# Kernel tuning notes

Measured on AMD Instinct MI355X. Metric: run time of the kernel, lower is better.

Reference implementation:

```python
import jax, jax.numpy as jnp
import numpy as np

EPS = 1e-6
SCALE_END = 1.0


def _rms_norm(x, w):
    # x: [B, L, H, D], w: [D]
    var = jnp.mean(jnp.square(x), axis=-1, keepdims=True)
    return x * jax.lax.rsqrt(var + EPS) * w


def _apply_rope(x, freqs):
    # x: [B, L, H, D]; freqs: [L, D//2] rotation angles.
    # Interleaved pair rotation: (x0, x1) -> (x0*cos - x1*sin, x0*sin + x1*cos)
    B, L, H, D = x.shape
    xr = x.reshape(B, L, H, D // 2, 2)
    x0, x1 = xr[..., 0], xr[..., 1]
    cos = jnp.cos(freqs)[None, :, None, :]  # [1, L, 1, D//2]
    sin = jnp.sin(freqs)[None, :, None, :]
    o0 = x0 * cos - x1 * sin
    o1 = x0 * sin + x1 * cos
    return jnp.stack([o0, o1], axis=-1).reshape(B, L, H, D)


def setup_inputs() -> dict:
    key = jax.random.key(0)
    ks = jax.random.split(key, 6)
    B, Lq, Lk, H, D = 1, 4096, 1024, 24, 128
    hidden = H * D
    query = jax.random.normal(ks[0], (B, Lq, H, D), dtype=jnp.float32)
    ref_latent = jax.random.normal(ks[1], (B, Lk, hidden), dtype=jnp.float32)
    ref_freqs = jax.random.uniform(ks[2], (Lk, D // 2), dtype=jnp.float32)
    Wk = jax.random.normal(ks[3], (hidden, hidden), dtype=jnp.float32) * (hidden ** -0.5)
    Wv = jax.random.normal(ks[4], (hidden, hidden), dtype=jnp.float32) * (hidden ** -0.5)
    rms_w = jnp.ones((D,), dtype=jnp.float32)
    return {"query": query, "ref_latent": ref_latent, "ref_freqs": ref_freqs,
            "Wk": Wk, "Wv": Wv, "rms_w": rms_w}


def reference(query, ref_latent, ref_freqs, Wk, Wv, rms_w):
    B, Lq, H, D = query.shape
    # K/V projections (nn.Linear: y = x @ W.T)
    ref_k = jnp.einsum('ble,he->blh', ref_latent, Wk).reshape(B, -1, H, D)
    ref_v = jnp.einsum('ble,he->blh', ref_latent, Wv).reshape(B, -1, H, D)
    # RMSNorm on K heads, then rotary embedding on K
    ref_k = _rms_norm(ref_k, rms_w)
    ref_k = _apply_rope(ref_k, ref_freqs)
    # Non-causal attention, softmax_scale = head_dim ** -0.5 (flash_attn layout B L H D)
    scale = D ** -0.5
    scores = jnp.einsum('bqhd,bkhd->bhqk', query, ref_k) * scale
    probs = jax.nn.softmax(scores, axis=-1)
    attn = jnp.einsum('bhqk,bkhd->bqhd', probs, ref_v)
    attn = attn.reshape(B, Lq, H * D)
    return SCALE_END * attn
```

## Files before the change

### kernel.cpp

```cpp
#include <hip/hip_runtime.h>
#include <hip/hip_bf16.h>

typedef __attribute__((ext_vector_type(8))) short short8;
typedef float floatx4 __attribute__((ext_vector_type(4)));
typedef float floatx16 __attribute__((ext_vector_type(16)));

#define LQ 4096
#define LK 1024
#define NH 24
#define HD 128
#define HID 3072

__device__ __forceinline__ unsigned short f2bf(float f) {
    __hip_bfloat16 h = __float2bfloat16(f);
    union { __hip_bfloat16 b; unsigned short u; } c; c.b = h;
    return c.u;
}

__device__ __forceinline__ unsigned cvtpk(float a, float b) {
    unsigned r;
    asm("v_cvt_pk_bf16_f32 %0, %1, %2" : "=v"(r) : "v"(a), "v"(b));
    return r;
}

__device__ __forceinline__ float fexp2(float x) {
    float r;
    asm("v_exp_f32 %0, %1" : "=v"(r) : "v"(x));
    return r;
}

__device__ __forceinline__ void gload16(const void* g, void* l) {
    __builtin_amdgcn_global_load_lds(
        (const __attribute__((address_space(1))) void*)g,
        (__attribute__((address_space(3))) void*)l,
        16, 0, 0);
}

__global__ void cvt_all(const float* __restrict__ latent, const float* __restrict__ Wk,
                        const float* __restrict__ Wv, unsigned short* __restrict__ lbf,
                        unsigned short* __restrict__ wkbf, unsigned short* __restrict__ wvbf) {
    const int n1 = (LK * HID) / 4;
    const int n2 = (HID * HID) / 4;
    const int total = n1 + 2 * n2;
    int i = blockIdx.x * blockDim.x + threadIdx.x;
    int stride = gridDim.x * blockDim.x;
    for (; i < total; i += stride) {
        const float4* src; ushort4* dst; int j;
        if (i < n1)            { src = (const float4*)latent; dst = (ushort4*)lbf;  j = i; }
        else if (i < n1 + n2)  { src = (const float4*)Wk;     dst = (ushort4*)wkbf; j = i - n1; }
        else                   { src = (const float4*)Wv;     dst = (ushort4*)wvbf; j = i - n1 - n2; }
        float4 v = src[j];
        ushort4 o;
        o.x = f2bf(v.x); o.y = f2bf(v.y); o.z = f2bf(v.z); o.w = f2bf(v.w);
        dst[j] = o;
    }
}

__global__ __launch_bounds__(256) void gemm_fused(const unsigned short* __restrict__ A,
                                                  const unsigned short* __restrict__ Bw,
                                                  const float* __restrict__ freqs,
                                                  const float* __restrict__ rmsw,
                                                  unsigned short* __restrict__ Out,
                                                  int mode) {
    __shared__ __align__(16) unsigned short As[2][32 * 64];
    __shared__ __align__(16) unsigned short Bs[2][128 * 64];
    __shared__ float redK[32][4];
    const int tid = threadIdx.x;
    const int lane = tid & 63;
    const int wave = tid >> 6;
    const int flat = blockIdx.x;
    const int wid = (flat & 7) * 96 + (flat >> 3);
    const int lt = wid & 31;
    const int h  = wid >> 5;
    const int bm0 = lt * 32;
    const int bn0 = h * 128;
    const int lr = lane & 15;
    const int lg = lane >> 4;

    floatx4 acc[2][2];
    for (int i = 0; i < 2; ++i)
        for (int j = 0; j < 2; ++j)
            acc[i][j] = (floatx4){0.f, 0.f, 0.f, 0.f};

    auto stage = [&](int b, int k0) {
        {
            int r = tid >> 3, cb = tid & 7;
            int g = cb ^ (r & 7);
            gload16(&A[(bm0 + r) * HID + k0 + g * 8], &As[b][(wave * 64) * 8]);
        }
        for (int p = 0; p < 4; ++p) {
            int slot = p * 256 + tid;
            int r = slot >> 3, cb = slot & 7;
            int g = cb ^ (r & 7);
            gload16(&Bw[(bn0 + r) * HID + k0 + g * 8], &Bs[b][(p * 256 + wave * 64) * 8]);
        }
    };

    auto compute = [&](int b) {
        for (int ks = 0; ks < 2; ++ks) {
            short8 af[2], bfr[2];
            for (int mt = 0; mt < 2; ++mt) {
                int m = mt * 16 + lr;
                int sc = (ks * 4 + lg) ^ (m & 7);
                af[mt] = *(const short8*)(&As[b][m * 64 + sc * 8]);
            }
            for (int nt = 0; nt < 2; ++nt) {
                int n = wave * 32 + nt * 16 + lr;
                int sc = (ks * 4 + lg) ^ (n & 7);
                bfr[nt] = *(const short8*)(&Bs[b][n * 64 + sc * 8]);
            }
            __builtin_amdgcn_s_setprio(1);
            for (int mt = 0; mt < 2; ++mt)
                for (int nt = 0; nt < 2; ++nt)
                    acc[mt][nt] = __builtin_amdgcn_mfma_f32_16x16x32_bf16(af[mt], bfr[nt], acc[mt][nt], 0, 0, 0);
            __builtin_amdgcn_s_setprio(0);
        }
    };

    stage(0, 0);
    __syncthreads();
    int buf = 0;
    for (int k0 = 0; k0 < HID - 64; k0 += 64) {
        stage(buf ^ 1, k0 + 64);
        compute(buf);
        __syncthreads();
        buf ^= 1;
    }
    compute(buf);

    if (mode == 0) {
        float part[2][4];
        for (int mt = 0; mt < 2; ++mt)
            for (int rg = 0; rg < 4; ++rg) {
                float v0 = acc[mt][0][rg], v1 = acc[mt][1][rg];
                float s = v0 * v0 + v1 * v1;
                s += __shfl_xor(s, 1);
                s += __shfl_xor(s, 2);
                s += __shfl_xor(s, 4);
                s += __shfl_xor(s, 8);
                part[mt][rg] = s;
            }
        if (lr == 0)
            for (int mt = 0; mt < 2; ++mt)
                for (int rg = 0; rg < 4; ++rg)
                    redK[mt * 16 + lg * 4 + rg][wave] = part[mt][rg];
        __syncthreads();
        for (int mt = 0; mt < 2; ++mt)
            for (int rg = 0; rg < 4; ++rg) {
                int row = mt * 16 + lg * 4 + rg;
                float tot = (redK[row][0] + redK[row][1]) + (redK[row][2] + redK[row][3]);
                float rsn = rsqrtf(tot * (1.0f / 128.0f) + 1e-6f);
                int l = bm0 + row;
                for (int nt = 0; nt < 2; ++nt) {
                    int d = wave * 32 + nt * 16 + lr;
                    float xn = acc[mt][nt][rg] * rsn * rmsw[d];
                    float f = freqs[l * (HD / 2) + (d >> 1)];
                    float sn = __sinf(f), cs = __cosf(f);
                    float partner = __shfl_xor(xn, 1);
                    float o = (d & 1) ? (partner * sn + xn * cs) : (xn * cs - partner * sn);
                    Out[l * HID + bn0 + d] = f2bf(o);
                }
            }
    } else {
        __syncthreads();
        float* Ct = (float*)&Bs[0][0];
        for (int mt = 0; mt < 2; ++mt)
            for (int nt = 0; nt < 2; ++nt)
                for (int rg = 0; rg < 4; ++rg)
                    Ct[(mt * 16 + lg * 4 + rg) * 132 + wave * 32 + nt * 16 + lr] = acc[mt][nt][rg];
        __syncthreads();
        unsigned short* dst = Out + (((size_t)(h * 32 + lt)) << 12);
        for (int p = 0; p < 2; ++p) {
            int slot = p * 256 + tid;
            int l31v = slot & 31;
            int hi2 = (slot >> 5) & 1;
            int c2 = (slot >> 6) & 1;
            int ntd = slot >> 7;
            int col = ntd * 32 + l31v;
            int r0 = c2 * 16 + hi2 * 8;
            short8 v;
            for (int j = 0; j < 8; ++j)
                v[j] = (short)f2bf(Ct[(r0 + j) * 132 + col]);
            *(short8*)(&dst[slot * 8]) = v;
        }
    }
}

__global__ __launch_bounds__(256, 3) void attn(const float* __restrict__ Q,
                                               const unsigned short* __restrict__ Kbf,
                                               const unsigned short* __restrict__ Vfrag,
                                               float* __restrict__ O) {
    __shared__ __align__(16) unsigned short KA[2][32 * 128];
    __shared__ __align__(16) unsigned short KB[2][32 * 128];
    __shared__ __align__(16) unsigned short VA[32 * 128];
    __shared__ __align__(16) unsigned short VB[32 * 128];
    const int tid = threadIdx.x;
    const int lane = tid & 63;
    const int wave = tid >> 6;
    const int l31 = lane & 31;
    const int hi = lane >> 5;
    const int flat = blockIdx.x + gridDim.x * blockIdx.y;
    const int wid = (flat & 7) * 96 + (flat >> 3);
    const int h = wid >> 5;
    const int q0 = (wid & 31) * 128 + wave * 32;
    const float qscale = 0.08838834764831843f * 1.44269504088896340736f;
    const float SHIFT = 32.0f;

    short8 qf[8];
#pragma unroll
    for (int m = 0; m < 8; ++m) {
        const float* qp = &Q[(q0 + l31) * HID + h * HD + m * 16 + hi * 8];
        float4 lo = *(const float4*)(qp);
        float4 hif = *(const float4*)(qp + 4);
        short8 v;
        v[0] = (short)f2bf(lo.x * qscale);
        v[1] = (short)f2bf(lo.y * qscale);
        v[2] = (short)f2bf(lo.z * qscale);
        v[3] = (short)f2bf(lo.w * qscale);
        v[4] = (short)f2bf(hif.x * qscale);
        v[5] = (short)f2bf(hif.y * qscale);
        v[6] = (short)f2bf(hif.z * qscale);
        v[7] = (short)f2bf(hif.w * qscale);
        qf[m] = v;
    }

    floatx16 accO[4];
#pragma unroll
    for (int i = 0; i < 4; ++i)
#pragma unroll
        for (int r = 0; r < 16; ++r) accO[i][r] = 0.f;
    float psum = 0.f;

    auto stageK = [&](unsigned short* dst, int kt) {
        for (int i = 0; i < 2; ++i) {
            int slot = i * 256 + tid;
            int r = slot >> 4, bb = slot & 15;
            int g = bb ^ (r & 15);
            gload16(&Kbf[(kt * 32 + r) * HID + h * HD + g * 8],
                    &dst[(i * 256 + wave * 64) * 8]);
        }
    };
    auto stageV = [&](unsigned short* dst, int kt) {
        const unsigned short* src = Vfrag + ((size_t)(h * 32 + kt) << 12);
        for (int i = 0; i < 2; ++i) {
            int slot = i * 256 + tid;
            gload16(&src[slot * 8], &dst[(i * 256 + wave * 64) * 8]);
        }
    };

    auto softmax32 = [&](floatx16 s, short8& pa, short8& pb) {
        float e[16];
#pragma unroll
        for (int r = 0; r < 16; ++r) e[r] = fexp2(s[r]);
        {
            float s01 = e[0] + e[1],   s23 = e[2] + e[3];
            float s45 = e[4] + e[5],   s67 = e[6] + e[7];
            float s89 = e[8] + e[9],   sab = e[10] + e[11];
            float scd = e[12] + e[13], sef = e[14] + e[15];
            float t0 = s01 + s23, t1 = s45 + s67, t2 = s89 + sab, t3 = scd + sef;
            psum += (t0 + t1) + (t2 + t3);
        }
        unsigned d0 = cvtpk(e[0], e[1]),   d1 = cvtpk(e[2], e[3]);
        unsigned d2 = cvtpk(e[4], e[5]),   d3 = cvtpk(e[6], e[7]);
        unsigned d4 = cvtpk(e[8], e[9]),   d5 = cvtpk(e[10], e[11]);
        unsigned d6 = cvtpk(e[12], e[13]), d7 = cvtpk(e[14], e[15]);
        asm volatile("v_permlane32_swap_b32 %0, %1" : "+v"(d0), "+v"(d2));
        asm volatile("v_permlane32_swap_b32 %0, %1" : "+v"(d1), "+v"(d3));
        asm volatile("v_permlane32_swap_b32 %0, %1" : "+v"(d4), "+v"(d6));
        asm volatile("v_permlane32_swap_b32 %0, %1" : "+v"(d5), "+v"(d7));
        union { unsigned u[4]; short8 s; } p0, p1;
        p0.u[0] = d0; p0.u[1] = d1; p0.u[2] = d2; p0.u[3] = d3;
        p1.u[0] = d4; p1.u[1] = d5; p1.u[2] = d6; p1.u[3] = d7;
        pa = p0.s; pb = p1.s;
    };

    stageK(KA[0], 0);
    stageK(KB[0], 16);
    asm volatile("s_waitcnt vmcnt(0)" ::: "memory");
    __builtin_amdgcn_s_barrier();

    for (int t = 0; t < 16; ++t) {
        stageV(VA, t);
        stageV(VB, t + 16);
        if (t < 15) {
            stageK(KA[(t + 1) & 1], t + 1);
            stageK(KB[(t + 1) & 1], t + 17);
        }
        floatx16 sA, sB;
#pragma unroll
        for (int r = 0; r < 16; ++r) { sA[r] = -SHIFT; sB[r] = -SHIFT; }
        __builtin_amdgcn_s_setprio(1);
#pragma unroll
        for (int m = 0; m < 8; ++m) {
            int slot = l31 * 16 + ((m * 2 + hi) ^ (l31 & 15));
            short8 kfa = *(const short8*)(&KA[t & 1][slot * 8]);
            short8 kfb = *(const short8*)(&KB[t & 1][slot * 8]);
            sA = __builtin_amdgcn_mfma_f32_32x32x16_bf16(kfa, qf[m], sA, 0, 0, 0);
            sB = __builtin_amdgcn_mfma_f32_32x32x16_bf16(kfb, qf[m], sB, 0, 0, 0);
        }
        __builtin_amdgcn_s_setprio(0);
        short8 pA0, pA1, pB0, pB1;
        softmax32(sA, pA0, pA1);
        softmax32(sB, pB0, pB1);
        __syncthreads();
        __builtin_amdgcn_s_setprio(1);
#pragma unroll
        for (int ntd = 0; ntd < 4; ++ntd) {
            int s0 = ((ntd * 2 + 0) * 2 + hi) * 32 + l31;
            int s1 = ((ntd * 2 + 1) * 2 + hi) * 32 + l31;
            short8 vA0 = *(const short8*)(&VA[s0 * 8]);
            short8 vA1 = *(const short8*)(&VA[s1 * 8]);
            short8 vB0 = *(const short8*)(&VB[s0 * 8]);
            short8 vB1 = *(const short8*)(&VB[s1 * 8]);
            accO[ntd] = __builtin_amdgcn_mfma_f32_32x32x16_bf16(pA0, vA0, accO[ntd], 0, 0, 0);
            accO[ntd] = __builtin_amdgcn_mfma_f32_32x32x16_bf16(pA1, vA1, accO[ntd], 0, 0, 0);
            accO[ntd] = __builtin_amdgcn_mfma_f32_32x32x16_bf16(pB0, vB0, accO[ntd], 0, 0, 0);
            accO[ntd] = __builtin_amdgcn_mfma_f32_32x32x16_bf16(pB1, vB1, accO[ntd], 0, 0, 0);
        }
        __builtin_amdgcn_s_setprio(0);
        __syncthreads();
    }

    float s = psum + __shfl_xor(psum, 32);
    float rinv = 1.0f / s;
    float ri[16];
#pragma unroll
    for (int r = 0; r < 16; ++r) {
        int row = (r & 3) + 8 * (r >> 2) + 4 * hi;
        ri[r] = __shfl(rinv, row);
    }
#pragma unroll
    for (int ntd = 0; ntd < 4; ++ntd)
#pragma unroll
        for (int r = 0; r < 16; ++r) {
            int row = (r & 3) + 8 * (r >> 2) + 4 * hi;
            O[(q0 + row) * HID + h * HD + ntd * 32 + l31] = accO[ntd][r] * ri[r];
        }
}

extern "C" void kernel_launch(void* const* d_in, const int* in_sizes, int n_in,
                              void* d_out, int out_size, void* d_ws, size_t ws_size,
                              hipStream_t stream) {
    const float* Q      = (const float*)d_in[0];
    const float* latent = (const float*)d_in[1];
    const float* freqs  = (const float*)d_in[2];
    const float* Wk     = (const float*)d_in[3];
    const float* Wv     = (const float*)d_in[4];
    const float* rmsw   = (const float*)d_in[5];
    float* out = (float*)d_out;
    char* ws = (char*)d_ws;

    unsigned short* latent_bf = (unsigned short*)(ws);
    unsigned short* Wk_bf     = (unsigned short*)(ws + 6291456);
    unsigned short* Wv_bf     = (unsigned short*)(ws + 25165824);
    unsigned short* Kbf       = (unsigned short*)(ws + 44040192);
    unsigned short* Vfrag     = (unsigned short*)(ws + 50331648);

    cvt_all<<<2048, 256, 0, stream>>>(latent, Wk, Wv, latent_bf, Wk_bf, Wv_bf);
    gemm_fused<<<768, 256, 0, stream>>>(latent_bf, Wk_bf, freqs, rmsw, Kbf, 0);
    gemm_fused<<<768, 256, 0, stream>>>(latent_bf, Wv_bf, freqs, rmsw, Vfrag, 1);
    attn<<<dim3(LQ / 128, NH), 256, 0, stream>>>(Q, Kbf, Vfrag, out);
}
```

Before: 163.8 us.

## Merge K and V projection GEMMs into one launch with 64x128 tiles

Replaces the two separate projection GEMM launches with a single kernel whose blockIdx.y selects the K or V weight. The block tile grows from 32x128 to 64x128, with a 2x2 wave layout where each wave computes 32x64, which raises arithmetic intensity per LDS load. The epilogues are adapted to the larger tile, and the V fragment store now writes two 32-row tiles. This cuts one launch and improves data reuse, at the cost of more LDS and registers per block and half as many blocks per projection.

Measured after the change: 134.6 us (median of 3 runs). 1.22x faster.

```diff
diff --git a/kernel.cpp b/kernel.cpp
--- a/kernel.cpp
+++ b/kernel.cpp
@@ -56,62 +56,69 @@
     }
 }
 
-__global__ __launch_bounds__(256) void gemm_fused(const unsigned short* __restrict__ A,
-                                                  const unsigned short* __restrict__ Bw,
+__global__ __launch_bounds__(256) void proj_fused(const unsigned short* __restrict__ A,
+                                                  const unsigned short* __restrict__ WkB,
+                                                  const unsigned short* __restrict__ WvB,
                                                   const float* __restrict__ freqs,
                                                   const float* __restrict__ rmsw,
-                                                  unsigned short* __restrict__ Out,
-                                                  int mode) {
-    __shared__ __align__(16) unsigned short As[2][32 * 64];
-    __shared__ __align__(16) unsigned short Bs[2][128 * 64];
-    __shared__ float redK[32][4];
+                                                  unsigned short* __restrict__ Kbf,
+                                                  unsigned short* __restrict__ Vfrag) {
+    __shared__ __align__(16) unsigned short sh[24576];
     const int tid = threadIdx.x;
     const int lane = tid & 63;
     const int wave = tid >> 6;
+    const int wm = wave >> 1, wn = wave & 1;
+    const int mode = blockIdx.y;
     const int flat = blockIdx.x;
-    const int wid = (flat & 7) * 96 + (flat >> 3);
-    const int lt = wid & 31;
-    const int h  = wid >> 5;
-    const int bm0 = lt * 32;
+    const int wid = (flat & 7) * 48 + (flat >> 3);
+    const int lt = wid & 15;
+    const int h  = wid >> 4;
+    const int bm0 = lt * 64;
     const int bn0 = h * 128;
     const int lr = lane & 15;
     const int lg = lane >> 4;
-
-    floatx4 acc[2][2];
+    const unsigned short* Bw = mode ? WvB : WkB;
+
+    floatx4 acc[2][4];
     for (int i = 0; i < 2; ++i)
-        for (int j = 0; j < 2; ++j)
+        for (int j = 0; j < 4; ++j)
             acc[i][j] = (floatx4){0.f, 0.f, 0.f, 0.f};
 
     auto stage = [&](int b, int k0) {
-        {
-            int r = tid >> 3, cb = tid & 7;
+        unsigned short* Asb = sh + b * 4096;
+        unsigned short* Bsb = sh + 8192 + b * 8192;
+        for (int p = 0; p < 2; ++p) {
+            int slot = p * 256 + tid;
+            int r = slot >> 3, cb = slot & 7;
             int g = cb ^ (r & 7);
-            gload16(&A[(bm0 + r) * HID + k0 + g * 8], &As[b][(wave * 64) * 8]);
+            gload16(&A[(bm0 + r) * HID + k0 + g * 8], &Asb[(p * 256 + wave * 64) * 8]);
         }
         for (int p = 0; p < 4; ++p) {
             int slot = p * 256 + tid;
             int r = slot >> 3, cb = slot & 7;
             int g = cb ^ (r & 7);
-            gload16(&Bw[(bn0 + r) * HID + k0 + g * 8], &Bs[b][(p * 256 + wave * 64) * 8]);
+            gload16(&Bw[(bn0 + r) * HID + k0 + g * 8], &Bsb[(p * 256 + wave * 64) * 8]);
         }
     };
 
     auto compute = [&](int b) {
+        const unsigned short* Asb = sh + b * 4096;
+        const unsigned short* Bsb = sh + 8192 + b * 8192;
         for (int ks = 0; ks < 2; ++ks) {
-            short8 af[2], bfr[2];
+            short8 af[2], bfr[4];
             for (int mt = 0; mt < 2; ++mt) {
-                int m = mt * 16 + lr;
+                int m = wm * 32 + mt * 16 + lr;
                 int sc = (ks * 4 + lg) ^ (m & 7);
-                af[mt] = *(const short8*)(&As[b][m * 64 + sc * 8]);
+                af[mt] = *(const short8*)(&Asb[m * 64 + sc * 8]);
             }
-            for (int nt = 0; nt < 2; ++nt) {
-                int n = wave * 32 + nt * 16 + lr;
+            for (int nt = 0; nt < 4; ++nt) {
+                int n = wn * 64 + nt * 16 + lr;
                 int sc = (ks * 4 + lg) ^ (n & 7);
-                bfr[nt] = *(const short8*)(&Bs[b][n * 64 + sc * 8]);
+                bfr[nt] = *(const short8*)(&Bsb[n * 64 + sc * 8]);
             }
             __builtin_amdgcn_s_setprio(1);
             for (int mt = 0; mt < 2; ++mt)
-                for (int nt = 0; nt < 2; ++nt)
+                for (int nt = 0; nt < 4; ++nt)
                     acc[mt][nt] = __builtin_amdgcn_mfma_f32_16x16x32_bf16(af[mt], bfr[nt], acc[mt][nt], 0, 0, 0);
             __builtin_amdgcn_s_setprio(0);
         }
@@ -127,61 +134,62 @@
         buf ^= 1;
     }
     compute(buf);
+    __syncthreads();
 
     if (mode == 0) {
-        float part[2][4];
+        float* red = (float*)sh;
         for (int mt = 0; mt < 2; ++mt)
             for (int rg = 0; rg < 4; ++rg) {
-                float v0 = acc[mt][0][rg], v1 = acc[mt][1][rg];
-                float s = v0 * v0 + v1 * v1;
+                float s = 0.f;
+                for (int nt = 0; nt < 4; ++nt) {
+                    float v = acc[mt][nt][rg];
+                    s += v * v;
+                }
                 s += __shfl_xor(s, 1);
                 s += __shfl_xor(s, 2);
                 s += __shfl_xor(s, 4);
                 s += __shfl_xor(s, 8);
-                part[mt][rg] = s;
+                if (lr == 0) red[(wm * 32 + mt * 16 + lg * 4 + rg) * 2 + wn] = s;
             }
-        if (lr == 0)
-            for (int mt = 0; mt < 2; ++mt)
-                for (int rg = 0; rg < 4; ++rg)
-                    redK[mt * 16 + lg * 4 + rg][wave] = part[mt][rg];
         __syncthreads();
         for (int mt = 0; mt < 2; ++mt)
             for (int rg = 0; rg < 4; ++rg) {
-                int row = mt * 16 + lg * 4 + rg;
-                float tot = (redK[row][0] + redK[row][1]) + (redK[row][2] + redK[row][3]);
+                int row = wm * 32 + mt * 16 + lg * 4 + rg;
+                float tot = red[row * 2] + red[row * 2 + 1];
                 float rsn = rsqrtf(tot * (1.0f / 128.0f) + 1e-6f);
                 int l = bm0 + row;
-                for (int nt = 0; nt < 2; ++nt) {
-                    int d = wave * 32 + nt * 16 + lr;
+                for (int nt = 0; nt < 4; ++nt) {
+                    int d = wn * 64 + nt * 16 + lr;
                     float xn = acc[mt][nt][rg] * rsn * rmsw[d];
                     float f = freqs[l * (HD / 2) + (d >> 1)];
                     float sn = __sinf(f), cs = __cosf(f);
                     float partner = __shfl_xor(xn, 1);
                     float o = (d & 1) ? (partner * sn + xn * cs) : (xn * cs - partner * sn);
-                    Out[l * HID + bn0 + d] = f2bf(o);
+                    Kbf[l * HID + bn0 + d] = f2bf(o);
                 }
             }
     } else {
-        __syncthreads();
-        float* Ct = (float*)&Bs[0][0];
+        float* Ct = (float*)sh;
         for (int mt = 0; mt < 2; ++mt)
-            for (int nt = 0; nt < 2; ++nt)
+            for (int nt = 0; nt < 4; ++nt)
                 for (int rg = 0; rg < 4; ++rg)
-                    Ct[(mt * 16 + lg * 4 + rg) * 132 + wave * 32 + nt * 16 + lr] = acc[mt][nt][rg];
-        __syncthreads();
-        unsigned short* dst = Out + (((size_t)(h * 32 + lt)) << 12);
-        for (int p = 0; p < 2; ++p) {
-            int slot = p * 256 + tid;
-            int l31v = slot & 31;
-            int hi2 = (slot >> 5) & 1;
-            int c2 = (slot >> 6) & 1;
-            int ntd = slot >> 7;
+                    Ct[(wm * 32 + mt * 16 + lg * 4 + rg) * 132 + wn * 64 + nt * 16 + lr] = acc[mt][nt][rg];
+        __syncthreads();
+        for (int p = 0; p < 4; ++p) {
+            int slot2 = p * 256 + tid;
+            int tile = slot2 >> 9;
+            int s = slot2 & 511;
+            int l31v = s & 31;
+            int hi2 = (s >> 5) & 1;
+            int c2 = (s >> 6) & 1;
+            int ntd = s >> 7;
             int col = ntd * 32 + l31v;
-            int r0 = c2 * 16 + hi2 * 8;
+            int r0 = tile * 32 + c2 * 16 + hi2 * 8;
             short8 v;
             for (int j = 0; j < 8; ++j)
                 v[j] = (short)f2bf(Ct[(r0 + j) * 132 + col]);
-            *(short8*)(&dst[slot * 8]) = v;
+            unsigned short* dst = Vfrag + (((size_t)(h * 32 + lt * 2 + tile)) << 12);
+            *(short8*)(&dst[s * 8]) = v;
         }
     }
 }
@@ -357,7 +365,6 @@
     unsigned short* Vfrag     = (unsigned short*)(ws + 50331648);
 
     cvt_all<<<2048, 256, 0, stream>>>(latent, Wk, Wv, latent_bf, Wk_bf, Wv_bf);
-    gemm_fused<<<768, 256, 0, stream>>>(latent_bf, Wk_bf, freqs, rmsw, Kbf, 0);
-    gemm_fused<<<768, 256, 0, stream>>>(latent_bf, Wv_bf, freqs, rmsw, Vfrag, 1);
+    proj_fused<<<dim3(384, 2), 256, 0, stream>>>(latent_bf, Wk_bf, Wv_bf, freqs, rmsw, Kbf, Vfrag);
     attn<<<dim3(LQ / 128, NH), 256, 0, stream>>>(Q, Kbf, Vfrag, out);
 }
```
